# Kernel tuning notes

Measured on AMD Instinct MI355X. Metric: run time of the kernel, lower is better.

The kernel has to match this reference:

```python
import jax, jax.numpy as jnp
import numpy as np

N_NODES = 40000
N_EDGES = 400000
N_GRAPHS = 128
IN_F = 768
HID = 128
HEADS = 4
NEG_SLOPE = 0.2  # DGL GATConv default


def _p(key, shape, scale=0.02):
    return jax.random.normal(key, shape, dtype=jnp.float32) * scale


def setup_inputs() -> dict:
    key = jax.random.key(0)
    ks = jax.random.split(key, 20)
    x = jax.random.normal(ks[0], (N_NODES, IN_F), dtype=jnp.float32)
    src = jax.random.randint(ks[1], (N_EDGES,), 0, N_NODES)
    dst = jax.random.randint(ks[2], (N_EDGES,), 0, N_NODES)
    graph_ids = jnp.sort(jax.random.randint(ks[3], (N_NODES,), 0, N_GRAPHS))
    params = {
        # GAT layer 1: 768 -> 4 heads x 128
        "W1": _p(ks[4], (IN_F, HEADS * HID)),
        "al1": _p(ks[5], (HEADS, HID)),
        "ar1": _p(ks[6], (HEADS, HID)),
        "b1": jnp.zeros((HEADS * HID,), jnp.float32),
        # GAT layer 2: 512 -> 1 head x 128
        "W2": _p(ks[7], (HEADS * HID, HID)),
        "al2": _p(ks[8], (1, HID)),
        "ar2": _p(ks[9], (1, HID)),
        "b2": jnp.zeros((HID,), jnp.float32),
        # node MLP: 128 -> 128 -> 2
        "nW1": _p(ks[10], (HID, HID)), "nb1": jnp.zeros((HID,), jnp.float32),
        "nW2": _p(ks[11], (HID, 2)), "nb2": jnp.zeros((2,), jnp.float32),
        # graph MLP: 128 -> 128 -> 2
        "gW1": _p(ks[12], (HID, HID)), "gb1": jnp.zeros((HID,), jnp.float32),
        "gW2": _p(ks[13], (HID, 2)), "gb2": jnp.zeros((2,), jnp.float32),
    }
    return dict(x=x, src=src, dst=dst, graph_ids=graph_ids, **params)


def gat_conv(h, W, attn_l, attn_r, bias, src, dst, heads, out_f):
    # DGL GATConv (eval mode, no dropout): project, per-edge attention logits,
    # segment softmax over incoming edges of each dst node, weighted scatter-add.
    feat = (h @ W).reshape(N_NODES, heads, out_f)           # [N,H,F]
    el = jnp.einsum('nhf,hf->nh', feat, attn_l)              # [N,H]
    er = jnp.einsum('nhf,hf->nh', feat, attn_r)              # [N,H]
    e = el[src] + er[dst]                                    # [E,H]
    e = jnp.where(e > 0, e, NEG_SLOPE * e)                   # LeakyReLU(0.2)
    emax = jax.ops.segment_max(e, dst, num_segments=N_NODES)  # [N,H], -inf for empty
    ee = jnp.exp(e - emax[dst])                              # [E,H]
    denom = jax.ops.segment_sum(ee, dst, num_segments=N_NODES)  # [N,H]
    alpha = ee / denom[dst]                                  # [E,H]
    msg = feat[src] * alpha[:, :, None]                      # [E,H,F]
    out = jax.ops.segment_sum(msg, dst, num_segments=N_NODES)  # [N,H,F]
    return out + bias.reshape(1, heads, out_f)


def reference(x, src, dst, graph_ids, W1, al1, ar1, b1, W2, al2, ar2, b2,
              nW1, nb1, nW2, nb2, gW1, gb1, gW2, gb2):
    h = gat_conv(x, W1, al1, ar1, b1, src, dst, HEADS, HID)   # [N,4,128]
    h = h.reshape(N_NODES, HEADS * HID)                       # flatten(1)
    h = gat_conv(h, W2, al2, ar2, b2, src, dst, 1, HID)       # [N,1,128]
    h = h.squeeze(1)                                          # [N,128]
    # dgl.mean_nodes over batched graphs
    cnt = jax.ops.segment_sum(jnp.ones((N_NODES,), h.dtype), graph_ids, num_segments=N_GRAPHS)
    hg = jax.ops.segment_sum(h, graph_ids, num_segments=N_GRAPHS) / jnp.maximum(cnt, 1.0)[:, None]
    node_logits = jax.nn.relu(h @ nW1 + nb1) @ nW2 + nb2      # [N,2]
    graph_logits = jax.nn.relu(hg @ gW1 + gb1) @ gW2 + gb2    # [G,2]
    return node_logits, graph_logits
```

## Files before the change

kernel.cpp:

```cpp
#include <hip/hip_runtime.h>
#include <cstddef>

#define NN 40000
#define NE 400000
#define NG 128
#define NB_SCAN 157

typedef __attribute__((ext_vector_type(8))) short bf16x8;
typedef __attribute__((ext_vector_type(4))) float f32x4;

__device__ __forceinline__ void split1(float x, unsigned short& h, unsigned short& l)
{
    unsigned u = __float_as_uint(x);
    unsigned rh = u + 0x7FFFu + ((u >> 16) & 1u);
    h = (unsigned short)(rh >> 16);
    float fh = __uint_as_float(((unsigned)h) << 16);
    float r = x - fh;
    unsigned u2 = __float_as_uint(r);
    unsigned rl = u2 + 0x7FFFu + ((u2 >> 16) & 1u);
    l = (unsigned short)(rl >> 16);
}

__global__ void conv_bt(const float* __restrict__ B, unsigned short* __restrict__ hi,
                        unsigned short* __restrict__ lo, int K, int N)
{
    int e = blockIdx.x * 256 + threadIdx.x;
    if (e >= K * N) return;
    int n = e / K, k = e - n * K;
    unsigned short h, l;
    split1(B[(size_t)k * N + n], h, l);
    hi[e] = h; lo[e] = l;
}

#define LDK 40

__global__ __launch_bounds__(256) void gemm_split(
    const float* __restrict__ A, const unsigned short* __restrict__ Bh,
    const unsigned short* __restrict__ Bl, float* __restrict__ C,
    int M, int K, int N, int swz)
{
    __shared__ unsigned short Ah_s[128 * LDK];
    __shared__ unsigned short Al_s[128 * LDK];
    __shared__ unsigned short Bh_s[128 * LDK];
    __shared__ unsigned short Bl_s[128 * LDK];

    int bm, bn;
    if (swz) {
        int xcd = blockIdx.x & 7;
        int loc = blockIdx.x >> 3;
        int bmi = xcd * 40 + (loc >> 2);
        if (bmi >= 313) return;
        bm = bmi * 128;
        bn = (loc & 3) * 128;
    } else {
        bm = blockIdx.x * 128;
        bn = blockIdx.y * 128;
    }

    const int t    = threadIdx.x;
    const int lane = t & 63;
    const int wid  = t >> 6;
    const int wr   = wid >> 1, wc = wid & 1;

    const int sr = t >> 1;
    const int sk = (t & 1) * 16;

    const int arow = bm + sr;
    const bool aval = (arow < M);
    const float* Ap = A + (size_t)arow * K + sk;
    const unsigned short* Bhp = Bh + (size_t)(bn + sr) * K + sk;
    const unsigned short* Blp = Bl + (size_t)(bn + sr) * K + sk;

    f32x4 acc[4][4];
    #pragma unroll
    for (int i = 0; i < 4; ++i)
        #pragma unroll
        for (int j = 0; j < 4; ++j) acc[i][j] = (f32x4){0.f, 0.f, 0.f, 0.f};

    float4 abuf[4];
    uint4 bhbuf[2], blbuf[2];
    const int NT = K / 32;

    auto load_tile = [&](int kt) {
        const int kb = kt * 32;
        if (aval) {
            #pragma unroll
            for (int q = 0; q < 4; ++q) abuf[q] = *(const float4*)(Ap + kb + q * 4);
        } else {
            #pragma unroll
            for (int q = 0; q < 4; ++q) abuf[q] = make_float4(0.f, 0.f, 0.f, 0.f);
        }
        bhbuf[0] = *(const uint4*)(Bhp + kb);
        bhbuf[1] = *(const uint4*)(Bhp + kb + 8);
        blbuf[0] = *(const uint4*)(Blp + kb);
        blbuf[1] = *(const uint4*)(Blp + kb + 8);
    };

    auto store_tile = [&]() {
        unsigned short h[16], l[16];
        #pragma unroll
        for (int q = 0; q < 4; ++q) {
            split1(abuf[q].x, h[q * 4 + 0], l[q * 4 + 0]);
            split1(abuf[q].y, h[q * 4 + 1], l[q * 4 + 1]);
            split1(abuf[q].z, h[q * 4 + 2], l[q * 4 + 2]);
            split1(abuf[q].w, h[q * 4 + 3], l[q * 4 + 3]);
        }
        *(uint4*)&Ah_s[sr * LDK + sk]     = *(uint4*)&h[0];
        *(uint4*)&Ah_s[sr * LDK + sk + 8] = *(uint4*)&h[8];
        *(uint4*)&Al_s[sr * LDK + sk]     = *(uint4*)&l[0];
        *(uint4*)&Al_s[sr * LDK + sk + 8] = *(uint4*)&l[8];
        *(uint4*)&Bh_s[sr * LDK + sk]     = bhbuf[0];
        *(uint4*)&Bh_s[sr * LDK + sk + 8] = bhbuf[1];
        *(uint4*)&Bl_s[sr * LDK + sk]     = blbuf[0];
        *(uint4*)&Bl_s[sr * LDK + sk + 8] = blbuf[1];
    };

    auto compute = [&]() {
        const int fr = lane & 15;
        const int fk = (lane >> 4) * 8;
        bf16x8 bhf[4], blf[4];
        #pragma unroll
        for (int ni = 0; ni < 4; ++ni) {
            bhf[ni] = *(bf16x8*)&Bh_s[(wc * 64 + ni * 16 + fr) * LDK + fk];
            blf[ni] = *(bf16x8*)&Bl_s[(wc * 64 + ni * 16 + fr) * LDK + fk];
        }
        #pragma unroll
        for (int mi = 0; mi < 4; ++mi) {
            bf16x8 ah = *(bf16x8*)&Ah_s[(wr * 64 + mi * 16 + fr) * LDK + fk];
            bf16x8 al = *(bf16x8*)&Al_s[(wr * 64 + mi * 16 + fr) * LDK + fk];
            #pragma unroll
            for (int ni = 0; ni < 4; ++ni) {
                acc[mi][ni] = __builtin_amdgcn_mfma_f32_16x16x32_bf16(ah, bhf[ni], acc[mi][ni], 0, 0, 0);
                acc[mi][ni] = __builtin_amdgcn_mfma_f32_16x16x32_bf16(ah, blf[ni], acc[mi][ni], 0, 0, 0);
                acc[mi][ni] = __builtin_amdgcn_mfma_f32_16x16x32_bf16(al, bhf[ni], acc[mi][ni], 0, 0, 0);
            }
        }
    };

    load_tile(0);
    store_tile();
    __syncthreads();
    for (int kt = 0;;) {
        if (kt + 1 < NT) load_tile(kt + 1);
        compute();
        ++kt;
        if (kt == NT) break;
        __syncthreads();
        store_tile();
        __syncthreads();
    }

    const int fr = lane & 15;
    const int fq = lane >> 4;
    #pragma unroll
    for (int mi = 0; mi < 4; ++mi) {
        int r0 = bm + wr * 64 + mi * 16 + fq * 4;
        #pragma unroll
        for (int ni = 0; ni < 4; ++ni) {
            int c = bn + wc * 64 + ni * 16 + fr;
            #pragma unroll
            for (int q = 0; q < 4; ++q) {
                int r = r0 + q;
                if (r < M) C[(size_t)r * N + c] = acc[mi][ni][q];
            }
        }
    }
}

__global__ void hist_kernel(const int* __restrict__ dst, int* __restrict__ cnt)
{
    int e = blockIdx.x * 256 + threadIdx.x;
    if (e < NE) atomicAdd(&cnt[dst[e]], 1);
}

__global__ __launch_bounds__(256) void scanA_kernel(
    const int* __restrict__ cnt, int* __restrict__ row, int* __restrict__ bsum)
{
    __shared__ int s[256];
    int t = threadIdx.x;
    int i = blockIdx.x * 256 + t;
    int v = (i < NN) ? cnt[i] : 0;
    s[t] = v;
    __syncthreads();
    #pragma unroll
    for (int off = 1; off < 256; off <<= 1) {
        int x = (t >= off) ? s[t - off] : 0;
        __syncthreads();
        s[t] += x;
        __syncthreads();
    }
    if (i < NN) row[i] = s[t] - v;
    if (t == 255) bsum[blockIdx.x] = s[255];
}

__global__ __launch_bounds__(256) void scanB_kernel(int* __restrict__ bsum)
{
    __shared__ int s[256];
    int t = threadIdx.x;
    int v = (t < NB_SCAN) ? bsum[t] : 0;
    s[t] = v;
    __syncthreads();
    #pragma unroll
    for (int off = 1; off < 256; off <<= 1) {
        int x = (t >= off) ? s[t - off] : 0;
        __syncthreads();
        s[t] += x;
        __syncthreads();
    }
    if (t < NB_SCAN) bsum[t] = s[t] - v;
}

__global__ void scanC_kernel(int* __restrict__ row, const int* __restrict__ bsum,
                             int* __restrict__ fill)
{
    int i = blockIdx.x * 256 + threadIdx.x;
    if (i < NN) {
        int r = row[i] + bsum[blockIdx.x];
        row[i] = r;
        fill[i] = r;
    }
    if (i == 0) row[NN] = NE;
}

__global__ void permute_kernel(const int* __restrict__ dst, int* __restrict__ fill,
                               int* __restrict__ eidx)
{
    int e = blockIdx.x * 256 + threadIdx.x;
    if (e < NE) {
        int pos = atomicAdd(&fill[dst[e]], 1);
        eidx[pos] = e;
    }
}

template <int H>
__global__ __launch_bounds__(256) void eler_kernel(
    const float* __restrict__ feat, const float* __restrict__ al,
    const float* __restrict__ ar, float* __restrict__ el, float* __restrict__ er)
{
    int wid  = (blockIdx.x * 256 + threadIdx.x) >> 6;
    int lane = threadIdx.x & 63;
    if (wid >= NN * H) return;
    int n = wid / H, h = wid % H;
    const float* f = feat + (size_t)n * (H * 128) + h * 128;
    float2 fv = *(const float2*)&f[lane * 2];
    float2 a1 = *(const float2*)&al[h * 128 + lane * 2];
    float2 a2 = *(const float2*)&ar[h * 128 + lane * 2];
    float sl = fv.x * a1.x + fv.y * a1.y;
    float sr = fv.x * a2.x + fv.y * a2.y;
    #pragma unroll
    for (int off = 32; off > 0; off >>= 1) {
        sl += __shfl_down(sl, off);
        sr += __shfl_down(sr, off);
    }
    if (lane == 0) { el[wid] = sl; er[wid] = sr; }
}

template <int H>
__global__ __launch_bounds__(256) void edge_w_kernel(
    const int* __restrict__ src, const int* __restrict__ dst,
    const float* __restrict__ el, const float* __restrict__ er,
    float* __restrict__ w)
{
    int e = blockIdx.x * 256 + threadIdx.x;
    if (e >= NE) return;
    int s = src[e], d = dst[e];
    if constexpr (H == 4) {
        float4 a = *(const float4*)&el[s * 4];
        float4 b = *(const float4*)&er[d * 4];
        float4 v = make_float4(a.x + b.x, a.y + b.y, a.z + b.z, a.w + b.w);
        v.x = v.x > 0.f ? v.x : 0.2f * v.x;
        v.y = v.y > 0.f ? v.y : 0.2f * v.y;
        v.z = v.z > 0.f ? v.z : 0.2f * v.z;
        v.w = v.w > 0.f ? v.w : 0.2f * v.w;
        *(float4*)&w[e * 4] = make_float4(__expf(v.x), __expf(v.y), __expf(v.z), __expf(v.w));
    } else {
        float v = el[s] + er[d];
        v = v > 0.f ? v : 0.2f * v;
        w[e] = __expf(v);
    }
}

template <int H>
__global__ __launch_bounds__(256) void agg_kernel(
    const int* __restrict__ row, const int* __restrict__ eidx,
    const int* __restrict__ src, const float* __restrict__ w,
    const float* __restrict__ feat, const float* __restrict__ bias,
    float* __restrict__ out)
{
    int wave = (blockIdx.x * 256 + threadIdx.x) >> 6;
    int lane = threadIdx.x & 63;
    if (wave >= NN) return;
    int r0 = row[wave], r1 = row[wave + 1];
    int nedge = r1 - r0;

    if constexpr (H == 4) {
        float d0 = 0.f, d1 = 0.f, d2 = 0.f, d3 = 0.f;
        float4 a0 = {0.f,0.f,0.f,0.f}, a1 = {0.f,0.f,0.f,0.f};
        for (int base = 0; base < nedge; base += 64) {
            int cnt = nedge - base; if (cnt > 64) cnt = 64;
            int s = 0;
            float4 wv = {0.f,0.f,0.f,0.f};
            if (lane < cnt) {
                int e = eidx[r0 + base + lane];
                s = src[e];
                wv = *(const float4*)&w[e * 4];
            }
            d0 += wv.x; d1 += wv.y; d2 += wv.z; d3 += wv.w;
            int j = 0;
            for (; j + 1 < cnt; j += 2) {
                int s0 = __shfl(s, j), s1 = __shfl(s, j + 1);
                float wx0 = __shfl(wv.x, j), wy0 = __shfl(wv.y, j);
                float wz0 = __shfl(wv.z, j), ww0 = __shfl(wv.w, j);
                float wx1 = __shfl(wv.x, j + 1), wy1 = __shfl(wv.y, j + 1);
                float wz1 = __shfl(wv.z, j + 1), ww1 = __shfl(wv.w, j + 1);
                const float* f0 = feat + (size_t)s0 * 512;
                const float* f1 = feat + (size_t)s1 * 512;
                float4 p00 = *(const float4*)&f0[lane * 4];
                float4 p01 = *(const float4*)&f0[256 + lane * 4];
                float4 p10 = *(const float4*)&f1[lane * 4];
                float4 p11 = *(const float4*)&f1[256 + lane * 4];
                float alo0 = (lane & 32) ? wy0 : wx0, ahi0 = (lane & 32) ? ww0 : wz0;
                float alo1 = (lane & 32) ? wy1 : wx1, ahi1 = (lane & 32) ? ww1 : wz1;
                a0.x = fmaf(p00.x, alo0, a0.x); a0.y = fmaf(p00.y, alo0, a0.y);
                a0.z = fmaf(p00.z, alo0, a0.z); a0.w = fmaf(p00.w, alo0, a0.w);
                a1.x = fmaf(p01.x, ahi0, a1.x); a1.y = fmaf(p01.y, ahi0, a1.y);
                a1.z = fmaf(p01.z, ahi0, a1.z); a1.w = fmaf(p01.w, ahi0, a1.w);
                a0.x = fmaf(p10.x, alo1, a0.x); a0.y = fmaf(p10.y, alo1, a0.y);
                a0.z = fmaf(p10.z, alo1, a0.z); a0.w = fmaf(p10.w, alo1, a0.w);
                a1.x = fmaf(p11.x, ahi1, a1.x); a1.y = fmaf(p11.y, ahi1, a1.y);
                a1.z = fmaf(p11.z, ahi1, a1.z); a1.w = fmaf(p11.w, ahi1, a1.w);
            }
            if (j < cnt) {
                int s0 = __shfl(s, j);
                float wx0 = __shfl(wv.x, j), wy0 = __shfl(wv.y, j);
                float wz0 = __shfl(wv.z, j), ww0 = __shfl(wv.w, j);
                const float* f0 = feat + (size_t)s0 * 512;
                float4 p00 = *(const float4*)&f0[lane * 4];
                float4 p01 = *(const float4*)&f0[256 + lane * 4];
                float alo0 = (lane & 32) ? wy0 : wx0, ahi0 = (lane & 32) ? ww0 : wz0;
                a0.x = fmaf(p00.x, alo0, a0.x); a0.y = fmaf(p00.y, alo0, a0.y);
                a0.z = fmaf(p00.z, alo0, a0.z); a0.w = fmaf(p00.w, alo0, a0.w);
                a1.x = fmaf(p01.x, ahi0, a1.x); a1.y = fmaf(p01.y, ahi0, a1.y);
                a1.z = fmaf(p01.z, ahi0, a1.z); a1.w = fmaf(p01.w, ahi0, a1.w);
            }
        }
        #pragma unroll
        for (int off = 32; off > 0; off >>= 1) {
            d0 += __shfl_xor(d0, off);
            d1 += __shfl_xor(d1, off);
            d2 += __shfl_xor(d2, off);
            d3 += __shfl_xor(d3, off);
        }
        float ilo = (lane & 32) ? d1 : d0;
        float ihi = (lane & 32) ? d3 : d2;
        ilo = (nedge > 0) ? 1.0f / ilo : 0.0f;
        ihi = (nedge > 0) ? 1.0f / ihi : 0.0f;
        float4 b0 = *(const float4*)&bias[lane * 4];
        float4 b1v = *(const float4*)&bias[256 + lane * 4];
        float* o = out + (size_t)wave * 512;
        *(float4*)&o[lane * 4] = make_float4(
            fmaf(a0.x, ilo, b0.x), fmaf(a0.y, ilo, b0.y),
            fmaf(a0.z, ilo, b0.z), fmaf(a0.w, ilo, b0.w));
        *(float4*)&o[256 + lane * 4] = make_float4(
            fmaf(a1.x, ihi, b1v.x), fmaf(a1.y, ihi, b1v.y),
            fmaf(a1.z, ihi, b1v.z), fmaf(a1.w, ihi, b1v.w));
    } else {
        float den = 0.f;
        float2 a = {0.f, 0.f};
        for (int base = 0; base < nedge; base += 64) {
            int cnt = nedge - base; if (cnt > 64) cnt = 64;
            int s = 0;
            float wv = 0.f;
            if (lane < cnt) {
                int e = eidx[r0 + base + lane];
                s = src[e];
                wv = w[e];
            }
            den += wv;
            int j = 0;
            for (; j + 1 < cnt; j += 2) {
                int s0 = __shfl(s, j), s1 = __shfl(s, j + 1);
                float w0 = __shfl(wv, j), w1 = __shfl(wv, j + 1);
                float2 p0 = *(const float2*)&feat[(size_t)s0 * 128 + lane * 2];
                float2 p1 = *(const float2*)&feat[(size_t)s1 * 128 + lane * 2];
                a.x = fmaf(p0.x, w0, a.x); a.y = fmaf(p0.y, w0, a.y);
                a.x = fmaf(p1.x, w1, a.x); a.y = fmaf(p1.y, w1, a.y);
            }
            if (j < cnt) {
                int s0 = __shfl(s, j);
                float w0 = __shfl(wv, j);
                float2 p0 = *(const float2*)&feat[(size_t)s0 * 128 + lane * 2];
                a.x = fmaf(p0.x, w0, a.x); a.y = fmaf(p0.y, w0, a.y);
            }
        }
        #pragma unroll
        for (int off = 32; off > 0; off >>= 1) den += __shfl_xor(den, off);
        float inv = (nedge > 0) ? 1.0f / den : 0.0f;
        float2 b = *(const float2*)&bias[lane * 2];
        float* o = out + (size_t)wave * 128;
        *(float2*)&o[lane * 2] = make_float2(fmaf(a.x, inv, b.x), fmaf(a.y, inv, b.y));
    }
}

__global__ __launch_bounds__(128) void graph_mean_kernel(
    const int* __restrict__ gid, const float* __restrict__ h2, float* __restrict__ hg)
{
    int g = blockIdx.x;
    int t = threadIdx.x;
    int lo = 0, hi = NN;
    while (lo < hi) { int m = (lo + hi) >> 1; if (gid[m] < g) lo = m + 1; else hi = m; }
    int start = lo;
    lo = start; hi = NN;
    while (lo < hi) { int m = (lo + hi) >> 1; if (gid[m] < g + 1) lo = m + 1; else hi = m; }
    int end = lo;
    float acc = 0.f;
    for (int n = start; n < end; ++n) acc += h2[(size_t)n * 128 + t];
    float c = fmaxf((float)(end - start), 1.0f);
    hg[g * 128 + t] = acc / c;
}

__global__ __launch_bounds__(128) void node_mlp_kernel(
    const float* __restrict__ h, const float* __restrict__ W1,
    const float* __restrict__ b1, const float* __restrict__ W2,
    const float* __restrict__ b2, float* __restrict__ out)
{
    __shared__ float row[128];
    __shared__ float hid[128];
    int n = blockIdx.x;
    int t = threadIdx.x;
    row[t] = h[(size_t)n * 128 + t];
    __syncthreads();
    float acc = b1[t];
    #pragma unroll 8
    for (int k = 0; k < 128; ++k) acc = fmaf(row[k], W1[k * 128 + t], acc);
    hid[t] = fmaxf(acc, 0.f);
    __syncthreads();
    if (t < 2) {
        float o = b2[t];
        for (int k = 0; k < 128; ++k) o = fmaf(hid[k], W2[k * 2 + t], o);
        out[(size_t)n * 2 + t] = o;
    }
}

__global__ __launch_bounds__(128) void graph_mlp_kernel(
    const float* __restrict__ hg,
    const float* __restrict__ W1, const float* __restrict__ b1,
    const float* __restrict__ W2, const float* __restrict__ b2,
    float* __restrict__ out)
{
    __shared__ float row[128];
    __shared__ float hid[128];
    int g = blockIdx.x;
    int t = threadIdx.x;
    row[t] = hg[(size_t)g * 128 + t];
    __syncthreads();
    float acc = b1[t];
    #pragma unroll 8
    for (int k = 0; k < 128; ++k) acc = fmaf(row[k], W1[k * 128 + t], acc);
    hid[t] = fmaxf(acc, 0.f);
    __syncthreads();
    if (t < 2) {
        float o = b2[t];
        for (int k = 0; k < 128; ++k) o = fmaf(hid[k], W2[k * 2 + t], o);
        out[(size_t)g * 2 + t] = o;
    }
}

static constexpr size_t O_FEAT1 = 0;
static constexpr size_t O_H1    = 20480000;
static constexpr size_t O_H2    = 5120000;
static constexpr size_t O_B2T   = 10240000;
static constexpr size_t O_EW    = 40960000;
static constexpr size_t O_HG    = 42880000;
static constexpr size_t O_INT   = 42896384;
static constexpr size_t I_ROW  = 0;
static constexpr size_t I_BSUM = 40064;
static constexpr size_t I_CNT  = 40224;
static constexpr size_t I_FILL = 80224;
static constexpr size_t I_EIDX = 120224;

extern "C" void kernel_launch(void* const* d_in, const int* in_sizes, int n_in,
                              void* d_out, int out_size, void* d_ws, size_t ws_size,
                              hipStream_t stream)
{
    const float* x    = (const float*)d_in[0];
    const int*   src  = (const int*)d_in[1];
    const int*   dst  = (const int*)d_in[2];
    const int*   gid  = (const int*)d_in[3];
    const float* W1   = (const float*)d_in[4];
    const float* al1  = (const float*)d_in[5];
    const float* ar1  = (const float*)d_in[6];
    const float* b1   = (const float*)d_in[7];
    const float* W2   = (const float*)d_in[8];
    const float* al2  = (const float*)d_in[9];
    const float* ar2  = (const float*)d_in[10];
    const float* b2   = (const float*)d_in[11];
    const float* nW1  = (const float*)d_in[12];
    const float* nb1  = (const float*)d_in[13];
    const float* nW2  = (const float*)d_in[14];
    const float* nb2  = (const float*)d_in[15];
    const float* gW1  = (const float*)d_in[16];
    const float* gb1  = (const float*)d_in[17];
    const float* gW2  = (const float*)d_in[18];
    const float* gb2  = (const float*)d_in[19];
    float* out = (float*)d_out;
    float* ws  = (float*)d_ws;

    float* feat1 = ws + O_FEAT1;
    float* h1    = ws + O_H1;
    float* feat2 = ws + O_FEAT1;
    float* h2    = ws + O_H2;
    float* el1   = ws + O_EW;
    float* er1   = ws + O_EW + 160000;
    float* w1e   = ws + O_EW + 320000;
    float* el2   = ws + O_EW;
    float* er2   = ws + O_EW + 40000;
    float* w2e   = ws + O_EW + 80000;
    float* hg    = ws + O_HG;
    int*   ibase = (int*)(ws + O_INT);
    int*   row   = ibase + I_ROW;
    int*   bsum  = ibase + I_BSUM;
    int*   cnt   = ibase + I_CNT;
    int*   fill  = ibase + I_FILL;
    int*   eidx  = ibase + I_EIDX;

    unsigned short* B1h = (unsigned short*)(ws + O_H1);
    unsigned short* B1l = B1h + 512 * 768;
    unsigned short* B2h = (unsigned short*)(ws + O_B2T);
    unsigned short* B2l = B2h + 128 * 512;

    hipMemsetAsync(cnt, 0, NN * sizeof(int), stream);
    hist_kernel<<<(NE + 255) / 256, 256, 0, stream>>>(dst, cnt);
    scanA_kernel<<<NB_SCAN, 256, 0, stream>>>(cnt, row, bsum);
    scanB_kernel<<<1, 256, 0, stream>>>(bsum);
    scanC_kernel<<<NB_SCAN, 256, 0, stream>>>(row, bsum, fill);
    permute_kernel<<<(NE + 255) / 256, 256, 0, stream>>>(dst, fill, eidx);

    conv_bt<<<(512 * 768 + 255) / 256, 256, 0, stream>>>(W1, B1h, B1l, 768, 512);
    gemm_split<<<1280, 256, 0, stream>>>(x, B1h, B1l, feat1, NN, 768, 512, 1);
    eler_kernel<4><<<(NN * 4 * 64 + 255) / 256, 256, 0, stream>>>(feat1, al1, ar1, el1, er1);
    edge_w_kernel<4><<<(NE + 255) / 256, 256, 0, stream>>>(src, dst, el1, er1, w1e);
    agg_kernel<4><<<10000, 256, 0, stream>>>(row, eidx, src, w1e, feat1, b1, h1);

    conv_bt<<<(128 * 512 + 255) / 256, 256, 0, stream>>>(W2, B2h, B2l, 512, 128);
    gemm_split<<<dim3(313, 1), 256, 0, stream>>>(h1, B2h, B2l, feat2, NN, 512, 128, 0);
    eler_kernel<1><<<(NN * 64 + 255) / 256, 256, 0, stream>>>(feat2, al2, ar2, el2, er2);
    edge_w_kernel<1><<<(NE + 255) / 256, 256, 0, stream>>>(src, dst, el2, er2, w2e);
    agg_kernel<1><<<10000, 256, 0, stream>>>(row, eidx, src, w2e, feat2, b2, h2);

    graph_mean_kernel<<<NG, 128, 0, stream>>>(gid, h2, hg);
    node_mlp_kernel<<<NN, 128, 0, stream>>>(h2, nW1, nb1, nW2, nb2, out);
    graph_mlp_kernel<<<NG, 128, 0, stream>>>(hg, gW1, gb1, gW2, gb2, out + (size_t)NN * 2);
}
```

Before: 940.8 us.

## Pre-split GEMM A operands into bf16 hi/lo, fusing layer-1 split into aggregation

Adds a gemm_ps kernel that reads A already split into bf16 hi/lo halves instead of splitting fp32 values inside the GEMM main loop. Layer-1 aggregation now writes its output directly as hi/lo bf16 pairs for the second GEMM, so the fp32 h1 buffer is never written or reread. When the workspace is large enough, x is pre-split by a separate conv_a pass before the first GEMM. The pre-split adds a full extra read and write of x (a 40000x768 fp32 input), which trades memory traffic for less ALU work in the GEMM, and it relies on the workspace size check.

```diff
diff --git a/kernel.cpp b/kernel.cpp
--- a/kernel.cpp
+++ b/kernel.cpp
@@ -32,12 +32,29 @@
     hi[e] = h; lo[e] = l;
 }
 
+__global__ __launch_bounds__(256) void conv_a(const float* __restrict__ A,
+                                              unsigned short* __restrict__ hi,
+                                              unsigned short* __restrict__ lo,
+                                              size_t total4)
+{
+    size_t i = ((size_t)blockIdx.x * 256 + threadIdx.x);
+    if (i >= total4) return;
+    float4 v = *(const float4*)&A[i * 4];
+    unsigned short h[4], l[4];
+    split1(v.x, h[0], l[0]);
+    split1(v.y, h[1], l[1]);
+    split1(v.z, h[2], l[2]);
+    split1(v.w, h[3], l[3]);
+    *(uint2*)&hi[i * 4] = *(const uint2*)&h[0];
+    *(uint2*)&lo[i * 4] = *(const uint2*)&l[0];
+}
+
 #define LDK 40
 
-__global__ __launch_bounds__(256) void gemm_split(
-    const float* __restrict__ A, const unsigned short* __restrict__ Bh,
-    const unsigned short* __restrict__ Bl, float* __restrict__ C,
-    int M, int K, int N, int swz)
+__global__ __launch_bounds__(256) void gemm_ps(
+    const unsigned short* __restrict__ Ahg, const unsigned short* __restrict__ Alg,
+    const unsigned short* __restrict__ Bh, const unsigned short* __restrict__ Bl,
+    float* __restrict__ C, int M, int K, int N, int swz)
 {
     __shared__ unsigned short Ah_s[128 * LDK];
     __shared__ unsigned short Al_s[128 * LDK];
@@ -61,7 +78,127 @@
     const int lane = t & 63;
     const int wid  = t >> 6;
     const int wr   = wid >> 1, wc = wid & 1;
-
+    const int sr = t >> 1;
+    const int sk = (t & 1) * 16;
+
+    const int arow = bm + sr;
+    const bool aval = (arow < M);
+    const unsigned short* Ahp = Ahg + (size_t)arow * K + sk;
+    const unsigned short* Alp = Alg + (size_t)arow * K + sk;
+    const unsigned short* Bhp = Bh + (size_t)(bn + sr) * K + sk;
+    const unsigned short* Blp = Bl + (size_t)(bn + sr) * K + sk;
+
+    f32x4 acc[4][4];
+    #pragma unroll
+    for (int i = 0; i < 4; ++i)
+        #pragma unroll
+        for (int j = 0; j < 4; ++j) acc[i][j] = (f32x4){0.f, 0.f, 0.f, 0.f};
+
+    uint4 ahb[2], alb[2], bhb[2], blb[2];
+    const int NT = K / 32;
+
+    auto load_tile = [&](int kt) {
+        const int kb = kt * 32;
+        if (aval) {
+            ahb[0] = *(const uint4*)(Ahp + kb); ahb[1] = *(const uint4*)(Ahp + kb + 8);
+            alb[0] = *(const uint4*)(Alp + kb); alb[1] = *(const uint4*)(Alp + kb + 8);
+        } else {
+            ahb[0] = ahb[1] = alb[0] = alb[1] = make_uint4(0, 0, 0, 0);
+        }
+        bhb[0] = *(const uint4*)(Bhp + kb); bhb[1] = *(const uint4*)(Bhp + kb + 8);
+        blb[0] = *(const uint4*)(Blp + kb); blb[1] = *(const uint4*)(Blp + kb + 8);
+    };
+
+    auto store_tile = [&]() {
+        *(uint4*)&Ah_s[sr * LDK + sk]     = ahb[0];
+        *(uint4*)&Ah_s[sr * LDK + sk + 8] = ahb[1];
+        *(uint4*)&Al_s[sr * LDK + sk]     = alb[0];
+        *(uint4*)&Al_s[sr * LDK + sk + 8] = alb[1];
+        *(uint4*)&Bh_s[sr * LDK + sk]     = bhb[0];
+        *(uint4*)&Bh_s[sr * LDK + sk + 8] = bhb[1];
+        *(uint4*)&Bl_s[sr * LDK + sk]     = blb[0];
+        *(uint4*)&Bl_s[sr * LDK + sk + 8] = blb[1];
+    };
+
+    auto compute = [&]() {
+        const int fr = lane & 15;
+        const int fk = (lane >> 4) * 8;
+        bf16x8 bhf[4], blf[4];
+        #pragma unroll
+        for (int ni = 0; ni < 4; ++ni) {
+            bhf[ni] = *(bf16x8*)&Bh_s[(wc * 64 + ni * 16 + fr) * LDK + fk];
+            blf[ni] = *(bf16x8*)&Bl_s[(wc * 64 + ni * 16 + fr) * LDK + fk];
+        }
+        #pragma unroll
+        for (int mi = 0; mi < 4; ++mi) {
+            bf16x8 ah = *(bf16x8*)&Ah_s[(wr * 64 + mi * 16 + fr) * LDK + fk];
+            bf16x8 al = *(bf16x8*)&Al_s[(wr * 64 + mi * 16 + fr) * LDK + fk];
+            #pragma unroll
+            for (int ni = 0; ni < 4; ++ni) {
+                acc[mi][ni] = __builtin_amdgcn_mfma_f32_16x16x32_bf16(ah, bhf[ni], acc[mi][ni], 0, 0, 0);
+                acc[mi][ni] = __builtin_amdgcn_mfma_f32_16x16x32_bf16(ah, blf[ni], acc[mi][ni], 0, 0, 0);
+                acc[mi][ni] = __builtin_amdgcn_mfma_f32_16x16x32_bf16(al, bhf[ni], acc[mi][ni], 0, 0, 0);
+            }
+        }
+    };
+
+    load_tile(0);
+    store_tile();
+    __syncthreads();
+    for (int kt = 0;;) {
+        if (kt + 1 < NT) load_tile(kt + 1);
+        compute();
+        ++kt;
+        if (kt == NT) break;
+        __syncthreads();
+        store_tile();
+        __syncthreads();
+    }
+
+    const int fr = lane & 15;
+    const int fq = lane >> 4;
+    #pragma unroll
+    for (int mi = 0; mi < 4; ++mi) {
+        int r0 = bm + wr * 64 + mi * 16 + fq * 4;
+        #pragma unroll
+        for (int ni = 0; ni < 4; ++ni) {
+            int c = bn + wc * 64 + ni * 16 + fr;
+            #pragma unroll
+            for (int q = 0; q < 4; ++q) {
+                int r = r0 + q;
+                if (r < M) C[(size_t)r * N + c] = acc[mi][ni][q];
+            }
+        }
+    }
+}
+
+__global__ __launch_bounds__(256) void gemm_split(
+    const float* __restrict__ A, const unsigned short* __restrict__ Bh,
+    const unsigned short* __restrict__ Bl, float* __restrict__ C,
+    int M, int K, int N, int swz)
+{
+    __shared__ unsigned short Ah_s[128 * LDK];
+    __shared__ unsigned short Al_s[128 * LDK];
+    __shared__ unsigned short Bh_s[128 * LDK];
+    __shared__ unsigned short Bl_s[128 * LDK];
+
+    int bm, bn;
+    if (swz) {
+        int xcd = blockIdx.x & 7;
+        int loc = blockIdx.x >> 3;
+        int bmi = xcd * 40 + (loc >> 2);
+        if (bmi >= 313) return;
+        bm = bmi * 128;
+        bn = (loc & 3) * 128;
+    } else {
+        bm = blockIdx.x * 128;
+        bn = blockIdx.y * 128;
+    }
+
+    const int t    = threadIdx.x;
+    const int lane = t & 63;
+    const int wid  = t >> 6;
+    const int wr   = wid >> 1, wc = wid & 1;
     const int sr = t >> 1;
     const int sk = (t & 1) * 16;
 
@@ -285,7 +422,8 @@
     const int* __restrict__ row, const int* __restrict__ eidx,
     const int* __restrict__ src, const float* __restrict__ w,
     const float* __restrict__ feat, const float* __restrict__ bias,
-    float* __restrict__ out)
+    float* __restrict__ out, unsigned short* __restrict__ oh,
+    unsigned short* __restrict__ ol)
 {
     int wave = (blockIdx.x * 256 + threadIdx.x) >> 6;
     int lane = threadIdx.x & 63;
@@ -357,13 +495,20 @@
         ihi = (nedge > 0) ? 1.0f / ihi : 0.0f;
         float4 b0 = *(const float4*)&bias[lane * 4];
         float4 b1v = *(const float4*)&bias[256 + lane * 4];
-        float* o = out + (size_t)wave * 512;
-        *(float4*)&o[lane * 4] = make_float4(
-            fmaf(a0.x, ilo, b0.x), fmaf(a0.y, ilo, b0.y),
-            fmaf(a0.z, ilo, b0.z), fmaf(a0.w, ilo, b0.w));
-        *(float4*)&o[256 + lane * 4] = make_float4(
-            fmaf(a1.x, ihi, b1v.x), fmaf(a1.y, ihi, b1v.y),
-            fmaf(a1.z, ihi, b1v.z), fmaf(a1.w, ihi, b1v.w));
+        float res[8];
+        res[0] = fmaf(a0.x, ilo, b0.x);  res[1] = fmaf(a0.y, ilo, b0.y);
+        res[2] = fmaf(a0.z, ilo, b0.z);  res[3] = fmaf(a0.w, ilo, b0.w);
+        res[4] = fmaf(a1.x, ihi, b1v.x); res[5] = fmaf(a1.y, ihi, b1v.y);
+        res[6] = fmaf(a1.z, ihi, b1v.z); res[7] = fmaf(a1.w, ihi, b1v.w);
+        unsigned short hh[8], ll[8];
+        #pragma unroll
+        for (int q = 0; q < 8; ++q) split1(res[q], hh[q], ll[q]);
+        size_t o0 = (size_t)wave * 512 + lane * 4;
+        size_t o1 = (size_t)wave * 512 + 256 + lane * 4;
+        *(uint2*)&oh[o0] = *(const uint2*)&hh[0];
+        *(uint2*)&oh[o1] = *(const uint2*)&hh[4];
+        *(uint2*)&ol[o0] = *(const uint2*)&ll[0];
+        *(uint2*)&ol[o1] = *(const uint2*)&ll[4];
     } else {
         float den = 0.f;
         float2 a = {0.f, 0.f};
@@ -478,6 +623,9 @@
 static constexpr size_t I_CNT  = 40224;
 static constexpr size_t I_FILL = 80224;
 static constexpr size_t I_EIDX = 120224;
+static constexpr size_t O_A1H  = 43420000;
+static constexpr size_t O_A1L  = 58780000;
+static constexpr size_t WS_NEEDED = 74140000ull * 4;
 
 extern "C" void kernel_launch(void* const* d_in, const int* in_sizes, int n_in,
                               void* d_out, int out_size, void* d_ws, size_t ws_size,
@@ -507,7 +655,6 @@
     float* ws  = (float*)d_ws;
 
     float* feat1 = ws + O_FEAT1;
-    float* h1    = ws + O_H1;
     float* feat2 = ws + O_FEAT1;
     float* h2    = ws + O_H2;
     float* el1   = ws + O_EW;
@@ -528,6 +675,11 @@
     unsigned short* B1l = B1h + 512 * 768;
     unsigned short* B2h = (unsigned short*)(ws + O_B2T);
     unsigned short* B2l = B2h + 128 * 512;
+    unsigned short* A2h = (unsigned short*)(ws + O_H1);
+    unsigned short* A2l = (unsigned short*)(ws + O_H1 + 10240000);
+    unsigned short* A1h = (unsigned short*)(ws + O_A1H);
+    unsigned short* A1l = (unsigned short*)(ws + O_A1L);
+    const bool presplit = (ws_size >= WS_NEEDED);
 
     hipMemsetAsync(cnt, 0, NN * sizeof(int), stream);
     hist_kernel<<<(NE + 255) / 256, 256, 0, stream>>>(dst, cnt);
@@ -537,16 +689,23 @@
     permute_kernel<<<(NE + 255) / 256, 256, 0, stream>>>(dst, fill, eidx);
 
     conv_bt<<<(512 * 768 + 255) / 256, 256, 0, stream>>>(W1, B1h, B1l, 768, 512);
-    gemm_split<<<1280, 256, 0, stream>>>(x, B1h, B1l, feat1, NN, 768, 512, 1);
+    if (presplit) {
+        conv_a<<<30000, 256, 0, stream>>>(x, A1h, A1l, (size_t)NN * 768 / 4);
+        gemm_ps<<<1280, 256, 0, stream>>>(A1h, A1l, B1h, B1l, feat1, NN, 768, 512, 1);
+    } else {
+        gemm_split<<<1280, 256, 0, stream>>>(x, B1h, B1l, feat1, NN, 768, 512, 1);
+    }
     eler_kernel<4><<<(NN * 4 * 64 + 255) / 256, 256, 0, stream>>>(feat1, al1, ar1, el1, er1);
     edge_w_kernel<4><<<(NE + 255) / 256, 256, 0, stream>>>(src, dst, el1, er1, w1e);
-    agg_kernel<4><<<10000, 256, 0, stream>>>(row, eidx, src, w1e, feat1, b1, h1);
+    agg_kernel<4><<<10000, 256, 0, stream>>>(row, eidx, src, w1e, feat1, b1,
+                                             nullptr, A2h, A2l);
 
     conv_bt<<<(128 * 512 + 255) / 256, 256, 0, stream>>>(W2, B2h, B2l, 512, 128);
-    gemm_split<<<dim3(313, 1), 256, 0, stream>>>(h1, B2h, B2l, feat2, NN, 512, 128, 0);
+    gemm_ps<<<dim3(313, 1), 256, 0, stream>>>(A2h, A2l, B2h, B2l, feat2, NN, 512, 128, 0);
     eler_kernel<1><<<(NN * 64 + 255) / 256, 256, 0, stream>>>(feat2, al2, ar2, el2, er2);
     edge_w_kernel<1><<<(NE + 255) / 256, 256, 0, stream>>>(src, dst, el2, er2, w2e);
-    agg_kernel<1><<<10000, 256, 0, stream>>>(row, eidx, src, w2e, feat2, b2, h2);
+    agg_kernel<1><<<10000, 256, 0, stream>>>(row, eidx, src, w2e, feat2, b2,
+                                             h2, nullptr, nullptr);
 
     graph_mean_kernel<<<NG, 128, 0, stream>>>(gid, h2, hg);
     node_mlp_kernel<<<NN, 128, 0, stream>>>(h2, nW1, nb1, nW2, nb2, out);
```

Result: slower. 982.0 us (+4.4%).
